# Optimization experiments

Measured on AMD Instinct MI355X. Metric: run time of the kernel, lower is better.

The kernel has to match this reference:

```python
import jax, jax.numpy as jnp
import numpy as np

B, T, C, H, MEM = 2, 2048, 1024, 16, 256
HD = C // H


def setup_inputs() -> dict:
    key = jax.random.key(0)
    ks = jax.random.split(key, 6)
    return {
        "x": jax.random.normal(ks[0], (B, T, C), dtype=jnp.float32),
        "ext_mem": jax.random.normal(ks[1], (B, MEM, C), dtype=jnp.float32),
        "W_attn": jax.random.normal(ks[2], (C, 3 * C), dtype=jnp.float32) * 0.02,
        "b_attn": jax.random.normal(ks[3], (3 * C,), dtype=jnp.float32) * 0.02,
        "W_proj": jax.random.normal(ks[4], (C, C), dtype=jnp.float32) * 0.02,
        "b_proj": jax.random.normal(ks[5], (C,), dtype=jnp.float32) * 0.02,
    }


def reference(x, ext_mem, W_attn, b_attn, W_proj, b_proj):
    Bx, Tx, Cx = x.shape
    qkv = x @ W_attn + b_attn                      # [B,T,3C]
    q, k, v = jnp.split(qkv, 3, axis=-1)
    # [B,H,T,HD]
    q = q.reshape(Bx, Tx, H, HD).transpose(0, 2, 1, 3)
    k = k.reshape(Bx, Tx, H, HD).transpose(0, 2, 1, 3)
    v = v.reshape(Bx, Tx, H, HD).transpose(0, 2, 1, 3)
    mem = ext_mem.reshape(Bx, -1, H, HD).transpose(0, 2, 1, 3)  # [B,H,MEM,HD]
    k = jnp.concatenate([mem, k], axis=2)          # [B,H,MEM+T,HD]
    v = jnp.concatenate([mem, v], axis=2)
    mem_len = k.shape[2] - Tx
    scale = 1.0 / jnp.sqrt(jnp.float32(HD))
    att = jnp.einsum("bhtd,bhsd->bhts", q, k) * scale  # [B,H,T,MEM+T]
    # memory prefix fully attended; causal over the T query positions
    rows = jnp.arange(Tx)[:, None]
    cols = jnp.arange(mem_len + Tx)[None, :]
    allowed = (cols < mem_len) | ((cols - mem_len) <= rows)  # [T,MEM+T]
    att = jnp.where(allowed[None, None], att, jnp.float32(-jnp.inf))
    att = jax.nn.softmax(att, axis=-1)
    y = jnp.einsum("bhts,bhsd->bhtd", att, v)      # [B,H,T,HD]
    y = y.transpose(0, 2, 1, 3).reshape(Bx, Tx, Cx)
    return y @ W_proj + b_proj
```

## Files before the change

### kernel.cpp

```cpp
#include <hip/hip_runtime.h>

#define B_    2
#define T_    2048
#define C_    1024
#define H_    16
#define HD_   64
#define MEM_  256
#define S_    2304
#define NKT_  36

typedef __attribute__((ext_vector_type(8))) short short8;
typedef __attribute__((ext_vector_type(4))) short short4v;
typedef __attribute__((ext_vector_type(4))) float f32x4;

__device__ __forceinline__ unsigned short f2bf(float x) {
    return (unsigned short)((__float_as_uint(x) + 0x8000u) >> 16);
}

__device__ __forceinline__ unsigned int pk2bf(float lo, float hi) {
    unsigned int a = __float_as_uint(lo) + 0x8000u;
    unsigned int b = __float_as_uint(hi) + 0x8000u;
    return __builtin_amdgcn_perm(b, a, 0x07060302);
}

typedef const __attribute__((address_space(1))) unsigned int* gp_t;
typedef __attribute__((address_space(3))) unsigned int* lp_t;

__device__ __forceinline__ void gll16(const unsigned short* g, unsigned short* l) {
    __builtin_amdgcn_global_load_lds((gp_t)g, (lp_t)l, 16, 0, 0);
}

#define C1_ 0.18033688011112042f

__global__ __launch_bounds__(256) void prep_all(
    const float* __restrict__ x, const float* __restrict__ Wa,
    const float* __restrict__ Wp, const float* __restrict__ ext,
    unsigned short* __restrict__ x_tl, unsigned short* __restrict__ WtA,
    unsigned short* __restrict__ WtP, unsigned short* __restrict__ k_ws,
    unsigned short* __restrict__ v_tl)
{
    __shared__ float L[64][65];
    const int bid = blockIdx.x, tid = threadIdx.x;
    if (bid < 4096) {
        int i = bid * 256 + tid;
        int c = (i & 255) * 4;
        int m = i >> 8;
        float4 v = ((const float4*)x)[i];
        ushort4 o;
        o.x = f2bf(v.x); o.y = f2bf(v.y); o.z = f2bf(v.z); o.w = f2bf(v.w);
        int mt = m >> 7, r = m & 127, kc = c >> 5, cc = c & 31;
        int p = (cc >> 3) ^ ((r >> 1) & 3);
        *(ushort4*)&x_tl[(((size_t)mt * 32 + kc) << 12) + (r << 5) + p * 8 + (cc & 7)] = o;
    } else if (bid < 5120) {
        const float* in; unsigned short* out; int Cc, r0, c0;
        if (bid < 4864) {
            int r = bid - 4096; in = Wa; out = WtA; Cc = 3 * C_;
            c0 = (r % 48) * 64; r0 = (r / 48) * 64;
        } else {
            int r = bid - 4864; in = Wp; out = WtP; Cc = C_;
            c0 = (r & 15) * 64; r0 = (r >> 4) * 64;
        }
        const int jj = tid >> 4;
        const int i4 = (tid & 15) * 4;
#pragma unroll
        for (int t = 0; t < 4; ++t) {
            int j = jj + t * 16;
            float4 v = *(const float4*)(in + (size_t)(r0 + j) * Cc + c0 + i4);
            L[i4 + 0][j] = v.x; L[i4 + 1][j] = v.y;
            L[i4 + 2][j] = v.z; L[i4 + 3][j] = v.w;
        }
        __syncthreads();
#pragma unroll
        for (int t = 0; t < 4; ++t) {
            int n = c0 + jj + t * 16;
            int k = r0 + i4;
            ushort4 o;
            o.x = f2bf(L[jj + t * 16][i4 + 0]); o.y = f2bf(L[jj + t * 16][i4 + 1]);
            o.z = f2bf(L[jj + t * 16][i4 + 2]); o.w = f2bf(L[jj + t * 16][i4 + 3]);
            int nt = n >> 7, r = n & 127, kc = k >> 5, cc = k & 31;
            int p = (cc >> 3) ^ ((r >> 1) & 3);
            *(ushort4*)&out[(((size_t)nt * 32 + kc) << 12) + (r << 5) + p * 8 + (cc & 7)] = o;
        }
    } else {
        int idx = (bid - 5120) * 256 + tid;
        float val = ext[idx];
        int c = idx & (C_ - 1), m = (idx >> 10) & (MEM_ - 1), b = idx >> 18;
        int h = c >> 6, d = c & 63;
        int bh = b * H_ + h;
        unsigned short bv = f2bf(val);
        k_ws[(size_t)bh * S_ * 64 + (size_t)m * 64 + (((d >> 3) ^ (m & 7)) << 3) + (d & 7)] = bv;
        int ts = m >> 6, key = m & 63;
        v_tl[(((size_t)bh * NKT_ + ts) * 64 + d) * 64 + (((key >> 3) ^ (d & 7)) << 3) + (key & 7)] = bv;
    }
}

__global__ __launch_bounds__(256) void qkv_gemm(
    const unsigned short* __restrict__ A,
    const unsigned short* __restrict__ Bt,
    const float* __restrict__ bias,
    unsigned short* __restrict__ q_ws,
    unsigned short* __restrict__ k_ws,
    unsigned short* __restrict__ v_tl)
{
    __shared__ __align__(16) unsigned short As[2][4096];
    __shared__ __align__(16) unsigned short Bs[2][4096];
    const int tid = threadIdx.x, lane = tid & 63, wave = tid >> 6;
    const int wr = wave >> 1, wc = wave & 1;
    const size_t abase = (size_t)blockIdx.y * 32 * 4096;
    const size_t bbase = (size_t)blockIdx.x * 32 * 4096;

    f32x4 acc[4][4];
#pragma unroll
    for (int i = 0; i < 4; ++i)
#pragma unroll
        for (int j = 0; j < 4; ++j) acc[i][j] = (f32x4){0.f, 0.f, 0.f, 0.f};

    auto stage = [&](int kc, int buf) {
        const unsigned short* ga = A + abase + (size_t)kc * 4096;
        const unsigned short* gb = Bt + bbase + (size_t)kc * 4096;
#pragma unroll
        for (int s = 0; s < 2; ++s) {
            int seg = wave + s * 4;
            gll16(ga + seg * 512 + lane * 8, &As[buf][seg * 512]);
            gll16(gb + seg * 512 + lane * 8, &Bs[buf][seg * 512]);
        }
    };

    stage(0, 0);
    __syncthreads();
    for (int kc = 0; kc < 32; ++kc) {
        if (kc + 1 < 32) stage(kc + 1, (kc + 1) & 1);
        const unsigned short* as = As[kc & 1];
        const unsigned short* bs = Bs[kc & 1];
        short8 af[4], bf4[4];
#pragma unroll
        for (int i = 0; i < 4; ++i) {
            int row = wr * 64 + i * 16 + (lane & 15);
            int ph = (lane >> 4) ^ ((row >> 1) & 3);
            af[i] = *(const short8*)&as[row * 32 + ph * 8];
        }
#pragma unroll
        for (int j = 0; j < 4; ++j) {
            int row = wc * 64 + j * 16 + (lane & 15);
            int ph = (lane >> 4) ^ ((row >> 1) & 3);
            bf4[j] = *(const short8*)&bs[row * 32 + ph * 8];
        }
#pragma unroll
        for (int i = 0; i < 4; ++i)
#pragma unroll
            for (int j = 0; j < 4; ++j)
                acc[i][j] = __builtin_amdgcn_mfma_f32_16x16x32_bf16(
                    af[i], bf4[j], acc[i][j], 0, 0, 0);
        __syncthreads();
    }

#pragma unroll
    for (int j = 0; j < 4; ++j) {
        int n = blockIdx.x * 128 + wc * 64 + j * 16 + (lane & 15);
        float bs = bias[n];
        int sel = n >> 10, h = (n >> 6) & 15, d = n & 63;
#pragma unroll
        for (int i = 0; i < 4; ++i) {
            int m = blockIdx.y * 128 + wr * 64 + i * 16 + (lane >> 4) * 4;
            int b = m >> 11, t0 = m & (T_ - 1);
            int bh = b * H_ + h;
            if (sel == 0) {
                size_t base = ((size_t)bh * T_ + t0) * 64 + d;
#pragma unroll
                for (int r = 0; r < 4; ++r)
                    q_ws[base + (size_t)r * 64] = f2bf((acc[i][j][r] + bs) * C1_);
            } else if (sel == 1) {
#pragma unroll
                for (int r = 0; r < 4; ++r) {
                    int s = MEM_ + t0 + r;
                    k_ws[(size_t)bh * S_ * 64 + (size_t)s * 64
                         + (((d >> 3) ^ (s & 7)) << 3) + (d & 7)] =
                        f2bf(acc[i][j][r] + bs);
                }
            } else {
                int s0 = MEM_ + t0, ts = s0 >> 6, key = s0 & 63;
                ushort4 pv;
                pv.x = f2bf(acc[i][j][0] + bs);
                pv.y = f2bf(acc[i][j][1] + bs);
                pv.z = f2bf(acc[i][j][2] + bs);
                pv.w = f2bf(acc[i][j][3] + bs);
                *(ushort4*)&v_tl[(((size_t)bh * NKT_ + ts) * 64 + d) * 64
                                 + (((key >> 3) ^ (d & 7)) << 3) + (key & 7)] = pv;
            }
        }
    }
}

__global__ __launch_bounds__(256) void proj_gemm(
    const unsigned short* __restrict__ A,
    const unsigned short* __restrict__ Bt,
    const float* __restrict__ bias,
    float* __restrict__ out)
{
    __shared__ __align__(16) unsigned short As[2][2048];
    __shared__ __align__(16) unsigned short Bs[2][4096];
    const int tid = threadIdx.x, lane = tid & 63, wave = tid >> 6;
    const int m64 = blockIdx.y;
    const size_t abase = ((size_t)(m64 >> 1) * 32) * 4096 + (size_t)(m64 & 1) * 2048;
    const size_t bbase = (size_t)blockIdx.x * 32 * 4096;

    f32x4 acc[4][2];
#pragma unroll
    for (int i = 0; i < 4; ++i)
#pragma unroll
        for (int j = 0; j < 2; ++j) acc[i][j] = (f32x4){0.f, 0.f, 0.f, 0.f};

    auto stage = [&](int kc, int buf) {
        const unsigned short* ga = A + abase + (size_t)kc * 4096;
        const unsigned short* gb = Bt + bbase + (size_t)kc * 4096;
        gll16(ga + wave * 512 + lane * 8, &As[buf][wave * 512]);
        gll16(gb + wave * 512 + lane * 8, &Bs[buf][wave * 512]);
        gll16(gb + (wave + 4) * 512 + lane * 8, &Bs[buf][(wave + 4) * 512]);
    };

    stage(0, 0);
    __syncthreads();
    for (int kc = 0; kc < 32; ++kc) {
        if (kc + 1 < 32) stage(kc + 1, (kc + 1) & 1);
        const unsigned short* as = As[kc & 1];
        const unsigned short* bs = Bs[kc & 1];
        short8 af[4], bf2[2];
#pragma unroll
        for (int i = 0; i < 4; ++i) {
            int row = i * 16 + (lane & 15);
            int ph = (lane >> 4) ^ ((row >> 1) & 3);
            af[i] = *(const short8*)&as[row * 32 + ph * 8];
        }
#pragma unroll
        for (int j = 0; j < 2; ++j) {
            int row = wave * 32 + j * 16 + (lane & 15);
            int ph = (lane >> 4) ^ ((row >> 1) & 3);
            bf2[j] = *(const short8*)&bs[row * 32 + ph * 8];
        }
#pragma unroll
        for (int i = 0; i < 4; ++i)
#pragma unroll
            for (int j = 0; j < 2; ++j)
                acc[i][j] = __builtin_amdgcn_mfma_f32_16x16x32_bf16(
                    af[i], bf2[j], acc[i][j], 0, 0, 0);
        __syncthreads();
    }

#pragma unroll
    for (int j = 0; j < 2; ++j) {
        int n = blockIdx.x * 128 + wave * 32 + j * 16 + (lane & 15);
        float bs = bias[n];
#pragma unroll
        for (int i = 0; i < 4; ++i) {
            int m = m64 * 64 + i * 16 + (lane >> 4) * 4;
#pragma unroll
            for (int r = 0; r < 4; ++r)
                out[(size_t)(m + r) * C_ + n] = acc[i][j][r] + bs;
        }
    }
}

__global__ __launch_bounds__(512, 4) void flash_mfma(
    const unsigned short* __restrict__ qg,
    const unsigned short* __restrict__ kg,
    const unsigned short* __restrict__ vg,
    unsigned short* __restrict__ yt)
{
    __shared__ __align__(16) unsigned short Ks[2][4096];
    __shared__ __align__(16) unsigned short Vs[2][4096];

    const int tid = threadIdx.x, lane = tid & 63, wave = tid >> 6;
    const int half = wave >> 2, wq = wave & 3;
    const int quad = lane >> 4;
    const int a = blockIdx.x;
    const int h = blockIdx.y, b = blockIdx.z;
    const int qt = half ? (31 - a) : a;
    const int nt = 5 + qt;
    const int ntMax = 36 - a;
    const int bh = b * H_ + h;
    const size_t kgb = (size_t)bh * S_ * 64;
    const size_t vgb = (size_t)bh * NKT_ * 4096;

    short8 qf[2];
    {
        const unsigned short* p = qg + ((size_t)bh * T_ + qt * 64 + wq * 16
                                        + (lane & 15)) * 64 + quad * 8;
        qf[0] = *(const short8*)p; qf[1] = *(const short8*)(p + 32);
    }

    f32x4 o[4];
#pragma unroll
    for (int j = 0; j < 4; ++j) o[j] = (f32x4){0.f, 0.f, 0.f, 0.f};
    float l = 0.f;

    const unsigned short* kB0 = &Ks[0][(lane & 15) * 64 + ((quad ^ (lane & 7)) * 8)];
    const unsigned short* kB1 = &Ks[0][(lane & 15) * 64 + (((quad + 4) ^ (lane & 7)) * 8)];
    const unsigned short* vPs[4];
#pragma unroll
    for (int kb = 0; kb < 4; ++kb)
        vPs[kb] = &Vs[0][(lane & 15) * 64
                         + (((kb * 2 + (lane >> 5)) ^ (lane & 7)) * 8)
                         + (quad & 1) * 4];

    auto stageTo = [&](int kt, int ofs) {
        const unsigned short* gk = kg + kgb + (size_t)kt * 4096;
        const unsigned short* gv = vg + vgb + (size_t)kt * 4096;
        gll16(gk + wave * 512 + lane * 8, &Ks[0][ofs + wave * 512]);
        gll16(gv + wave * 512 + lane * 8, &Vs[0][ofs + wave * 512]);
    };

    const int tq = qt * 64 + wq * 16 + (lane & 15);

    stageTo(0, 0);
    __syncthreads();
    for (int kt = 0; kt < ntMax; ++kt) {
        const int B = (kt & 1) << 12;
        if (kt + 1 < ntMax) stageTo(kt + 1, B ^ 4096);
        if (kt < nt) {
            const bool diag = (kt == nt - 1);
            const int s0 = kt * 64;
            short8 kA[4][2];
#pragma unroll
            for (int kb = 0; kb < 4; ++kb) {
                kA[kb][0] = *(const short8*)&kB0[B + kb * 1024];
                kA[kb][1] = *(const short8*)&kB1[B + kb * 1024];
            }
            short4v vF[4][4];
#pragma unroll
            for (int kb = 0; kb < 4; ++kb)
#pragma unroll
                for (int dblk = 0; dblk < 4; ++dblk)
                    vF[kb][dblk] = *(const short4v*)&vPs[kb][B + dblk * 1024];

#pragma unroll
            for (int kb = 0; kb < 4; ++kb) {
                f32x4 z = (f32x4){0.f, 0.f, 0.f, 0.f};
                z = __builtin_amdgcn_mfma_f32_16x16x32_bf16(kA[kb][0], qf[0], z, 0, 0, 0);
                z = __builtin_amdgcn_mfma_f32_16x16x32_bf16(kA[kb][1], qf[1], z, 0, 0, 0);
                float p[4];
#pragma unroll
                for (int r = 0; r < 4; ++r) {
                    float e = exp2f(z[r]);
                    if (diag) {
                        int key = s0 + kb * 16 + quad * 4 + r;
                        if (key - MEM_ > tq) e = 0.f;
                    }
                    l += e;
                    p[r] = e;
                }
                unsigned int r01 = pk2bf(p[0], p[1]);
                unsigned int r23 = pk2bf(p[2], p[3]);
                short4v pf;
                *(unsigned int*)&pf = r01;
                *((unsigned int*)&pf + 1) = r23;
#pragma unroll
                for (int dblk = 0; dblk < 4; ++dblk)
                    o[dblk] = __builtin_amdgcn_mfma_f32_16x16x16bf16_1k(
                        pf, vF[kb][dblk], o[dblk], 0, 0, 0);
            }
        }
        __syncthreads();
    }

    l += __shfl_xor(l, 16);
    l += __shfl_xor(l, 32);
    float linv[4];
#pragma unroll
    for (int r = 0; r < 4; ++r)
        linv[r] = 1.f / __shfl(l, quad * 4 + r);
#pragma unroll
    for (int dblk = 0; dblk < 4; ++dblk) {
        int c = h * 64 + dblk * 16 + (lane & 15);
        int kc = c >> 5, cc = c & 31;
#pragma unroll
        for (int r = 0; r < 4; ++r) {
            int t = qt * 64 + wq * 16 + quad * 4 + r;
            int m = b * T_ + t;
            int mt = m >> 7, rr = m & 127;
            int p = (cc >> 3) ^ ((rr >> 1) & 3);
            yt[(((size_t)mt * 32 + kc) << 12) + (rr << 5) + p * 8 + (cc & 7)] =
                f2bf(o[dblk][r] * linv[r]);
        }
    }
}

extern "C" void kernel_launch(void* const* d_in, const int* in_sizes, int n_in,
                              void* d_out, int out_size, void* d_ws, size_t ws_size,
                              hipStream_t stream) {
    (void)in_sizes; (void)n_in; (void)out_size; (void)ws_size;
    const float* x      = (const float*)d_in[0];
    const float* ext    = (const float*)d_in[1];
    const float* W_attn = (const float*)d_in[2];
    const float* b_attn = (const float*)d_in[3];
    const float* W_proj = (const float*)d_in[4];
    const float* b_proj = (const float*)d_in[5];
    float* out = (float*)d_out;

    unsigned short* x_tl  = (unsigned short*)d_ws;
    unsigned short* WtA   = x_tl + 4194304;
    unsigned short* WtP   = WtA + 3145728;
    unsigned short* q_ws  = WtP + 1048576;
    unsigned short* k_ws  = q_ws + 4194304;
    unsigned short* v_tl  = k_ws + 4718592;
    unsigned short* y_tl  = v_tl + 4718592;

    dim3 blk(256);
    prep_all<<<7168, blk, 0, stream>>>(x, W_attn, W_proj, ext,
                                       x_tl, WtA, WtP, k_ws, v_tl);
    qkv_gemm<<<dim3(24, 32), blk, 0, stream>>>(
        x_tl, WtA, b_attn, q_ws, k_ws, v_tl);
    flash_mfma<<<dim3(16, H_, B_), dim3(512), 0, stream>>>(q_ws, k_ws, v_tl, y_tl);
    proj_gemm<<<dim3(8, 64), blk, 0, stream>>>(y_tl, WtP, b_proj, out);
}
```

Before: 207.1 us.

## Split long causal row's KV tiles across both wave groups and merge partial sums

The flash attention block pairs a short and a long query tile. Previously the short-tile group sat idle while the long tile finished. Now, once the short group is done, it takes alternate KV tiles of the long query tile, and the partial outputs and row sums are merged through shared memory at the end. This balances work between the two wave groups. It also deepens the KV staging ring from 2 to 4 buffers, at the cost of more LDS, extra registers for a second accumulator and Q fragment, and a reduction step.

After: 195.5 us. -5.6%, faster.

```diff
diff --git a/kernel.cpp b/kernel.cpp
--- a/kernel.cpp
+++ b/kernel.cpp
@@ -266,32 +266,39 @@
     const unsigned short* __restrict__ vg,
     unsigned short* __restrict__ yt)
 {
-    __shared__ __align__(16) unsigned short Ks[2][4096];
-    __shared__ __align__(16) unsigned short Vs[2][4096];
-
-    const int tid = threadIdx.x, lane = tid & 63, wave = tid >> 6;
-    const int half = wave >> 2, wq = wave & 3;
+    __shared__ __align__(16) unsigned short Ks[4][4096];
+    __shared__ __align__(16) unsigned short Vs[4][4096];
+
+    const int tid = threadIdx.x, lane = tid & 63, w = tid >> 6;
+    const int grp = w >> 2, wq = w & 3;
     const int quad = lane >> 4;
     const int a = blockIdx.x;
     const int h = blockIdx.y, b = blockIdx.z;
-    const int qt = half ? (31 - a) : a;
-    const int nt = 5 + qt;
-    const int ntMax = 36 - a;
+    const int p0 = 5 + a;
+    const int nl = 36 - a;
+    const int n2 = nl - p0;
+    const int qt = grp ? (31 - a) : a;
     const int bh = b * H_ + h;
     const size_t kgb = (size_t)bh * S_ * 64;
     const size_t vgb = (size_t)bh * NKT_ * 4096;
 
-    short8 qf[2];
+    short8 qfP[2], qf2[2];
     {
         const unsigned short* p = qg + ((size_t)bh * T_ + qt * 64 + wq * 16
                                         + (lane & 15)) * 64 + quad * 8;
-        qf[0] = *(const short8*)p; qf[1] = *(const short8*)(p + 32);
-    }
-
-    f32x4 o[4];
-#pragma unroll
-    for (int j = 0; j < 4; ++j) o[j] = (f32x4){0.f, 0.f, 0.f, 0.f};
-    float l = 0.f;
+        qfP[0] = *(const short8*)p; qfP[1] = *(const short8*)(p + 32);
+        const unsigned short* q2 = qg + ((size_t)bh * T_ + (31 - a) * 64 + wq * 16
+                                         + (lane & 15)) * 64 + quad * 8;
+        qf2[0] = *(const short8*)q2; qf2[1] = *(const short8*)(q2 + 32);
+    }
+
+    f32x4 o[4], o2[4];
+#pragma unroll
+    for (int j = 0; j < 4; ++j) {
+        o[j] = (f32x4){0.f, 0.f, 0.f, 0.f};
+        o2[j] = (f32x4){0.f, 0.f, 0.f, 0.f};
+    }
+    float l = 0.f, l2 = 0.f;
 
     const unsigned short* kB0 = &Ks[0][(lane & 15) * 64 + ((quad ^ (lane & 7)) * 8)];
     const unsigned short* kB1 = &Ks[0][(lane & 15) * 64 + (((quad + 4) ^ (lane & 7)) * 8)];
@@ -302,64 +309,99 @@
                          + (((kb * 2 + (lane >> 5)) ^ (lane & 7)) * 8)
                          + (quad & 1) * 4];
 
-    auto stageTo = [&](int kt, int ofs) {
+    auto stageTo = [&](int kt) {
+        const int bf = kt & 3;
         const unsigned short* gk = kg + kgb + (size_t)kt * 4096;
         const unsigned short* gv = vg + vgb + (size_t)kt * 4096;
-        gll16(gk + wave * 512 + lane * 8, &Ks[0][ofs + wave * 512]);
-        gll16(gv + wave * 512 + lane * 8, &Vs[0][ofs + wave * 512]);
+        gll16(gk + w * 512 + lane * 8, &Ks[bf][w * 512]);
+        gll16(gv + w * 512 + lane * 8, &Vs[bf][w * 512]);
     };
 
-    const int tq = qt * 64 + wq * 16 + (lane & 15);
-
-    stageTo(0, 0);
+    const int tqP = qt * 64 + wq * 16 + (lane & 15);
+    const int tq2 = (31 - a) * 64 + wq * 16 + (lane & 15);
+
+    auto computeTile = [&](int kt, const short8 (&qf)[2], f32x4 (&oo)[4],
+                           float& ll, bool diag, int tq) {
+        const int B = (kt & 3) << 12;
+        const int s0 = kt * 64;
+        short8 kA[4][2];
+#pragma unroll
+        for (int kb = 0; kb < 4; ++kb) {
+            kA[kb][0] = *(const short8*)&kB0[B + kb * 1024];
+            kA[kb][1] = *(const short8*)&kB1[B + kb * 1024];
+        }
+        short4v vF[4][4];
+#pragma unroll
+        for (int kb = 0; kb < 4; ++kb)
+#pragma unroll
+            for (int dblk = 0; dblk < 4; ++dblk)
+                vF[kb][dblk] = *(const short4v*)&vPs[kb][B + dblk * 1024];
+
+#pragma unroll
+        for (int kb = 0; kb < 4; ++kb) {
+            f32x4 z = (f32x4){0.f, 0.f, 0.f, 0.f};
+            z = __builtin_amdgcn_mfma_f32_16x16x32_bf16(kA[kb][0], qf[0], z, 0, 0, 0);
+            z = __builtin_amdgcn_mfma_f32_16x16x32_bf16(kA[kb][1], qf[1], z, 0, 0, 0);
+            float p[4];
+#pragma unroll
+            for (int r = 0; r < 4; ++r) {
+                float e = exp2f(z[r]);
+                if (diag) {
+                    int key = s0 + kb * 16 + quad * 4 + r;
+                    if (key - MEM_ > tq) e = 0.f;
+                }
+                ll += e;
+                p[r] = e;
+            }
+            short4v pf;
+            *(unsigned int*)&pf       = pk2bf(p[0], p[1]);
+            *((unsigned int*)&pf + 1) = pk2bf(p[2], p[3]);
+#pragma unroll
+            for (int dblk = 0; dblk < 4; ++dblk)
+                oo[dblk] = __builtin_amdgcn_mfma_f32_16x16x16bf16_1k(
+                    pf, vF[kb][dblk], oo[dblk], 0, 0, 0);
+        }
+    };
+
+    stageTo(0); stageTo(1); stageTo(2);
+    int cursor = 3;
+
+    for (int s = 0; s < p0; ++s) {
+        __syncthreads();
+        computeTile(s, qfP, o, l, (grp == 0) && (s == p0 - 1), tqP);
+        if (cursor < nl && cursor <= s + 3) { stageTo(cursor); ++cursor; }
+    }
+
+    const int nsteps2 = (n2 + 1) >> 1;
+    for (int s2 = 0; s2 < nsteps2; ++s2) {
+        __syncthreads();
+        int t = p0 + 2 * s2 + grp;
+        if (t < nl) {
+            bool dg = (t == nl - 1);
+            if (grp == 0) computeTile(t, qf2, o2, l2, dg, tq2);
+            else          computeTile(t, qfP, o, l, dg, tqP);
+        }
+        while (cursor < nl && cursor <= p0 + 2 * s2 + 3) { stageTo(cursor); ++cursor; }
+    }
+
     __syncthreads();
-    for (int kt = 0; kt < ntMax; ++kt) {
-        const int B = (kt & 1) << 12;
-        if (kt + 1 < ntMax) stageTo(kt + 1, B ^ 4096);
-        if (kt < nt) {
-            const bool diag = (kt == nt - 1);
-            const int s0 = kt * 64;
-            short8 kA[4][2];
-#pragma unroll
-            for (int kb = 0; kb < 4; ++kb) {
-                kA[kb][0] = *(const short8*)&kB0[B + kb * 1024];
-                kA[kb][1] = *(const short8*)&kB1[B + kb * 1024];
-            }
-            short4v vF[4][4];
-#pragma unroll
-            for (int kb = 0; kb < 4; ++kb)
-#pragma unroll
-                for (int dblk = 0; dblk < 4; ++dblk)
-                    vF[kb][dblk] = *(const short4v*)&vPs[kb][B + dblk * 1024];
-
-#pragma unroll
-            for (int kb = 0; kb < 4; ++kb) {
-                f32x4 z = (f32x4){0.f, 0.f, 0.f, 0.f};
-                z = __builtin_amdgcn_mfma_f32_16x16x32_bf16(kA[kb][0], qf[0], z, 0, 0, 0);
-                z = __builtin_amdgcn_mfma_f32_16x16x32_bf16(kA[kb][1], qf[1], z, 0, 0, 0);
-                float p[4];
-#pragma unroll
-                for (int r = 0; r < 4; ++r) {
-                    float e = exp2f(z[r]);
-                    if (diag) {
-                        int key = s0 + kb * 16 + quad * 4 + r;
-                        if (key - MEM_ > tq) e = 0.f;
-                    }
-                    l += e;
-                    p[r] = e;
-                }
-                unsigned int r01 = pk2bf(p[0], p[1]);
-                unsigned int r23 = pk2bf(p[2], p[3]);
-                short4v pf;
-                *(unsigned int*)&pf = r01;
-                *((unsigned int*)&pf + 1) = r23;
-#pragma unroll
-                for (int dblk = 0; dblk < 4; ++dblk)
-                    o[dblk] = __builtin_amdgcn_mfma_f32_16x16x16bf16_1k(
-                        pf, vF[kb][dblk], o[dblk], 0, 0, 0);
-            }
-        }
-        __syncthreads();
+    float* sm = (float*)&Ks[0][0];
+    if (grp == 0) {
+        int idx = (wq * 64 + lane) * 17;
+#pragma unroll
+        for (int dblk = 0; dblk < 4; ++dblk)
+#pragma unroll
+            for (int r = 0; r < 4; ++r) sm[idx + dblk * 4 + r] = o2[dblk][r];
+        sm[idx + 16] = l2;
+    }
+    __syncthreads();
+    if (grp == 1) {
+        int idx = (wq * 64 + lane) * 17;
+#pragma unroll
+        for (int dblk = 0; dblk < 4; ++dblk)
+#pragma unroll
+            for (int r = 0; r < 4; ++r) o[dblk][r] += sm[idx + dblk * 4 + r];
+        l += sm[idx + 16];
     }
 
     l += __shfl_xor(l, 16);
```
